# Performance work log

Measured on AMD Instinct MI355X. Metric: run time of the kernel, lower is better.

## Reference

```python
import jax, jax.numpy as jnp
import numpy as np

D = 128      # internal_dimensions
L = 4        # num_edge_convs
N = 100000   # nodes
E = 800000   # edges
G = 64       # graphs
IN = 4       # in_channels


def _ln(x, g, b):
    m = jnp.mean(x, -1, keepdims=True)
    v = jnp.mean((x - m) ** 2, -1, keepdims=True)
    return (x - m) * jax.lax.rsqrt(v + 1e-5) * g + b


def _gelu(x):
    return jax.nn.gelu(x, approximate=False)  # torch nn.GELU default (erf)


def _seg_mean(x, seg, n):
    s = jax.ops.segment_sum(x, seg, num_segments=n)
    c = jax.ops.segment_sum(jnp.ones((x.shape[0], 1), x.dtype), seg, num_segments=n)
    return s / jnp.maximum(c, 1.0)


def _seg_max(x, seg, n):
    m = jax.ops.segment_max(x, seg, num_segments=n)
    return jnp.where(jnp.isfinite(m), m, 0.0)  # empty segments -> 0 (PyG convention)


def _forward(x, edge_index, batch, num_graphs,
             in_W1, in_b1, in_g1, in_bn1, in_W2, in_b2, in_g2, in_bn2,
             pre_g, pre_b, cW1, cb1, cg1, cbb1, cW2, cb2, cg2, cbb2, pW, pb,
             ag_g, ag_b,
             kW1, kb1, kg1, kbb1, kW2, kb2, kg2, kbb2,
             kW3, kb3, kg3, kbb3, kW4, kb4):
    n = x.shape[0]
    # input_net: Linear -> LN -> GELU -> Linear -> LN   (dropout=0, eval)
    h = _gelu(_ln(x @ in_W1 + in_b1, in_g1, in_bn1))
    h = _ln(h @ in_W2 + in_b2, in_g2, in_bn2)

    x_in_max = _seg_max(h, batch, num_graphs)
    x_in_mean = _seg_mean(h, batch, num_graphs)

    src, dst = edge_index[0], edge_index[1]  # PyG: message from src (x_j) to dst (x_i)
    xcur = h
    for l in range(L):
        identity = xcur
        hn = _ln(xcur, pre_g[l], pre_b[l])
        xi = hn[dst]            # [E, D]
        xj = hn[src]            # [E, D]
        m = jnp.concatenate([xi, xj - xi], axis=-1)       # [E, 2D]
        m = _gelu(_ln(m @ cW1[l] + cb1[l], cg1[l], cbb1[l]))
        m = _gelu(_ln(m @ cW2[l] + cb2[l], cg2[l], cbb2[l]))
        a_max = _seg_max(m, dst, n)
        a_mean = _seg_mean(m, dst, n)
        aggr = jnp.concatenate([a_max, a_mean], axis=-1)  # [N, 2D]
        xcur = identity + aggr @ pW[l] + pb[l]

    xcur = _ln(xcur, ag_g, ag_b)
    x_g_max = _seg_max(xcur, batch, num_graphs)
    x_g_mean = _seg_mean(xcur, batch, num_graphs)

    xp = jnp.concatenate([x_in_max, x_in_mean, x_g_max, x_g_mean], axis=-1)  # [G, 4D]
    z = _gelu(_ln(xp @ kW1 + kb1, kg1, kbb1))
    z = _gelu(_ln(z @ kW2 + kb2, kg2, kbb2))
    z = _gelu(_ln(z @ kW3 + kb3, kg3, kbb3))
    return z @ kW4 + kb4  # [G, 1]


def setup_inputs() -> dict:
    key = jax.random.key(0)
    ks = iter(jax.random.split(key, 64))
    def W(shape, fan):
        return jax.random.normal(next(ks), shape, jnp.float32) * np.float32((2.0 / fan) ** 0.5)
    inp = {}
    inp["x"] = jax.random.normal(next(ks), (N, IN), jnp.float32)
    inp["edge_index"] = jax.random.randint(next(ks), (2, E), 0, N)
    inp["batch"] = jnp.sort(jax.random.randint(next(ks), (N,), 0, G))
    inp["num_graphs"] = G
    inp["in_W1"] = W((IN, D), IN); inp["in_b1"] = jnp.zeros((D,), jnp.float32)
    inp["in_g1"] = jnp.ones((D,), jnp.float32); inp["in_bn1"] = jnp.zeros((D,), jnp.float32)
    inp["in_W2"] = W((D, D), D); inp["in_b2"] = jnp.zeros((D,), jnp.float32)
    inp["in_g2"] = jnp.ones((D,), jnp.float32); inp["in_bn2"] = jnp.zeros((D,), jnp.float32)
    inp["pre_g"] = jnp.ones((L, D), jnp.float32); inp["pre_b"] = jnp.zeros((L, D), jnp.float32)
    inp["cW1"] = W((L, 2 * D, D), 2 * D); inp["cb1"] = jnp.zeros((L, D), jnp.float32)
    inp["cg1"] = jnp.ones((L, D), jnp.float32); inp["cbb1"] = jnp.zeros((L, D), jnp.float32)
    inp["cW2"] = W((L, D, D), D); inp["cb2"] = jnp.zeros((L, D), jnp.float32)
    inp["cg2"] = jnp.ones((L, D), jnp.float32); inp["cbb2"] = jnp.zeros((L, D), jnp.float32)
    inp["pW"] = W((L, 2 * D, D), 2 * D); inp["pb"] = jnp.zeros((L, D), jnp.float32)
    inp["ag_g"] = jnp.ones((D,), jnp.float32); inp["ag_b"] = jnp.zeros((D,), jnp.float32)
    inp["kW1"] = W((4 * D, D), 4 * D); inp["kb1"] = jnp.zeros((D,), jnp.float32)
    inp["kg1"] = jnp.ones((D,), jnp.float32); inp["kbb1"] = jnp.zeros((D,), jnp.float32)
    inp["kW2"] = W((D, D), D); inp["kb2"] = jnp.zeros((D,), jnp.float32)
    inp["kg2"] = jnp.ones((D,), jnp.float32); inp["kbb2"] = jnp.zeros((D,), jnp.float32)
    inp["kW3"] = W((D, D // 4), D); inp["kb3"] = jnp.zeros((D // 4,), jnp.float32)
    inp["kg3"] = jnp.ones((D // 4,), jnp.float32); inp["kbb3"] = jnp.zeros((D // 4,), jnp.float32)
    inp["kW4"] = W((D // 4, 1), D // 4); inp["kb4"] = jnp.zeros((1,), jnp.float32)
    return inp


def reference(x, edge_index, batch, num_graphs,
              in_W1, in_b1, in_g1, in_bn1, in_W2, in_b2, in_g2, in_bn2,
              pre_g, pre_b, cW1, cb1, cg1, cbb1, cW2, cb2, cg2, cbb2, pW, pb,
              ag_g, ag_b,
              kW1, kb1, kg1, kbb1, kW2, kb2, kg2, kbb2,
              kW3, kb3, kg3, kbb3, kW4, kb4):
    return _forward(x, edge_index, batch, num_graphs,
                    in_W1, in_b1, in_g1, in_bn1, in_W2, in_b2, in_g2, in_bn2,
                    pre_g, pre_b, cW1, cb1, cg1, cbb1, cW2, cb2, cg2, cbb2, pW, pb,
                    ag_g, ag_b,
                    kW1, kb1, kg1, kbb1, kW2, kb2, kg2, kbb2,
                    kW3, kb3, kg3, kbb3, kW4, kb4)
```

## Files before the change

kernel.cpp:

```cpp
#include <hip/hip_runtime.h>
#include <hip/hip_bf16.h>
#include <math.h>

__device__ __forceinline__ float geluf(float x) {
    return 0.5f * x * (1.0f + erff(x * 0.70710678118654752f));
}
#define MAPNEGINF 0x007FFFFFu
__device__ __forceinline__ float funmap(unsigned m) {
    return __uint_as_float((m & 0x80000000u) ? (m ^ 0x80000000u) : ~m);
}
__device__ __forceinline__ unsigned fmap(float f) {
    unsigned u = __float_as_uint(f);
    return ((int)u < 0) ? ~u : (u | 0x80000000u);
}
__device__ __forceinline__ float wred64(float v) {
#pragma unroll
    for (int m = 1; m < 64; m <<= 1) v += __shfl_xor(v, m);
    return v;
}
__device__ __forceinline__ unsigned short bf16r(float f) {
    unsigned u = __float_as_uint(f);
    u += 0x7fffu + ((u >> 16) & 1u);
    return (unsigned short)(u >> 16);
}
// ... 35 lines not shown
__global__ void k_zero(unsigned* __restrict__ p, int n) {
    const int i = blockIdx.x * 256 + threadIdx.x;
    if (i < n) p[i] = 0u;
}

__global__ void k_copyu(const unsigned* __restrict__ a, const unsigned* __restrict__ b,
                        unsigned* __restrict__ ac, unsigned* __restrict__ bc, int n) {
    const int i = blockIdx.x * 256 + threadIdx.x;
    if (i < n) {
        ac[i] = a[i];
        bc[i] = b[i];
    }
}

__global__ void k_count(const int* __restrict__ ei, unsigned* __restrict__ deg, int E) {
    const int e = blockIdx.x * 256 + threadIdx.x;
    if (e < E) atomicAdd(deg + ei[E + e], 1u);
}

__global__ void k_scan1(const unsigned* __restrict__ deg, unsigned* __restrict__ excl,
                        unsigned* __restrict__ bsum, int n) {
    __shared__ unsigned sh[256];
    const int t = threadIdx.x;
    const int base = blockIdx.x * 1024 + t * 4;
    unsigned v0 = (base + 0 < n) ? deg[base + 0] : 0u;
    unsigned v1 = (base + 1 < n) ? deg[base + 1] : 0u;
    unsigned v2 = (base + 2 < n) ? deg[base + 2] : 0u;
    unsigned v3 = (base + 3 < n) ? deg[base + 3] : 0u;
    const unsigned s = v0 + v1 + v2 + v3;
    sh[t] = s;
    __syncthreads();
    for (int off = 1; off < 256; off <<= 1) {
        unsigned x = 0;
        if (t >= off) x = sh[t - off];
        __syncthreads();
        if (t >= off) sh[t] += x;
        __syncthreads();
    }
    const unsigned ebase = sh[t] - s;
    if (base + 0 < n) excl[base + 0] = ebase;
    if (base + 1 < n) excl[base + 1] = ebase + v0;
    if (base + 2 < n) excl[base + 2] = ebase + v0 + v1;
    if (base + 3 < n) excl[base + 3] = ebase + v0 + v1 + v2;
    if (t == 255) bsum[blockIdx.x] = sh[255];
}

__global__ void k_scan2(unsigned* __restrict__ bsum, int nb) {
    __shared__ unsigned sh[256];
    const int t = threadIdx.x;
    const unsigned v = (t < nb) ? bsum[t] : 0u;
    sh[t] = v;
    __syncthreads();
    for (int off = 1; off < 256; off <<= 1) {
        unsigned x = 0;
        if (t >= off) x = sh[t - off];
        __syncthreads();
        if (t >= off) sh[t] += x;
        __syncthreads();
    }
    if (t < nb) bsum[t] = sh[t] - v;
}

__global__ void k_scan3(unsigned* __restrict__ excl, const unsigned* __restrict__ bsum, int n) {
    const int t = threadIdx.x;
    const int base = blockIdx.x * 1024 + t * 4;
    const unsigned add = bsum[blockIdx.x];
#pragma unroll
    for (int j = 0; j < 4; ++j)
        if (base + j < n) excl[base + j] += add;
}

__global__ void k_scatter(const int* __restrict__ ei, unsigned* __restrict__ cursor,
                          int* __restrict__ esrc, int* __restrict__ edst, int E) {
    const int e = blockIdx.x * 256 + threadIdx.x;
    if (e < E) {
        const int s = ei[e];
        const int d = ei[E + e];
        const unsigned pos = atomicAdd(cursor + d, 1u);
        esrc[pos] = s;
        edst[pos] = d;
    }
}

__global__ void k_in1(const float* __restrict__ x, const float* __restrict__ W1,
                      const float* __restrict__ b1, const float* __restrict__ g1,
                      const float* __restrict__ bn1, float* __restrict__ h, int n) {
    const int t = threadIdx.x, lane = t & 63, wave = t >> 6;
    const int d0 = lane << 1;
    const float2 w0 = *(const float2*)(W1 + d0);
    const float2 w1 = *(const float2*)(W1 + 128 + d0);
    const float2 w2 = *(const float2*)(W1 + 256 + d0);
    const float2 w3 = *(const float2*)(W1 + 384 + d0);
    const float2 bb = *(const float2*)(b1 + d0);
    const float2 gg = *(const float2*)(g1 + d0);
    const float2 nn = *(const float2*)(bn1 + d0);
    const int stride = gridDim.x * 4;
    for (int node = blockIdx.x * 4 + wave; node < n; node += stride) {
        const float4 xv = *(const float4*)(x + (size_t)node * 4);
        float h0 = bb.x + xv.x * w0.x + xv.y * w1.x + xv.z * w2.x + xv.w * w3.x;
        float h1 = bb.y + xv.x * w0.y + xv.y * w1.y + xv.z * w2.y + xv.w * w3.y;
        const float s = wred64(h0 + h1), q = wred64(h0 * h0 + h1 * h1);
        const float mean = s * 0.0078125f, var = q * 0.0078125f - mean * mean;
        const float rs = rsqrtf(var + 1e-5f);
        h0 = geluf((h0 - mean) * rs * gg.x + nn.x);
        h1 = geluf((h1 - mean) * rs * gg.y + nn.y);
        *(float2*)(h + (size_t)node * 128 + d0) = make_float2(h0, h1);
    }
}

__global__ __launch_bounds__(256, 2) void k_in2(const float* __restrict__ A,
                                                const float* __restrict__ W,
                                                const float* __restrict__ bias,
                                                const float* __restrict__ g,
                                                const float* __restrict__ b,
                                                float* __restrict__ C, int n) {
    __shared__ float As[64 * 132];
    __shared__ float Ws[4096];
    const int t = threadIdx.x;
    const int n0 = blockIdx.x * 64;
    {
        const int r = t >> 2, c0 = (t & 3) << 5;
        const int row = n0 + r;
        const bool ok = row < n;
#pragma unroll
        for (int j = 0; j < 8; ++j) {
            const int col = c0 + (j << 2);
            float4 v = make_float4(0.f, 0.f, 0.f, 0.f);
            if (ok) v = *(const float4*)(A + (size_t)row * 128 + col);
            *(float4*)(As + r * 132 + col) = v;
        }
    }
    float acc[4][8];
#pragma unroll
    for (int r = 0; r < 4; ++r)
#pragma unroll
        for (int o = 0; o < 8; ++o) acc[r][o] = 0.f;
    const int og = t & 15, eg = t >> 4;
    const int ogc = og << 2, r0 = eg << 2;
#pragma unroll
    for (int q4 = 0; q4 < 4; ++q4) {
        stage_wq(Ws, W + q4 * 4096, t);
        __syncthreads();
        kloop_q(As, Ws, acc, r0, ogc, q4 * 32);
        __syncthreads();
    }
    const float4 bA = *(const float4*)(bias + ogc);
    const float4 bB = *(const float4*)(bias + 64 + ogc);
    const float4 gA = *(const float4*)(g + ogc);
    const float4 gB = *(const float4*)(g + 64 + ogc);
    const float4 lA = *(const float4*)(b + ogc);
    const float4 lB = *(const float4*)(b + 64 + ogc);
#pragma unroll
    for (int r = 0; r < 4; ++r) {
        float v[8];
        v[0] = acc[r][0] + bA.x; v[1] = acc[r][1] + bA.y;
        v[2] = acc[r][2] + bA.z; v[3] = acc[r][3] + bA.w;
        v[4] = acc[r][4] + bB.x; v[5] = acc[r][5] + bB.y;
        v[6] = acc[r][6] + bB.z; v[7] = acc[r][7] + bB.w;
        float s = 0.f, q = 0.f;
#pragma unroll
        for (int o = 0; o < 8; ++o) { s += v[o]; q += v[o] * v[o]; }
#pragma unroll
        for (int m = 1; m < 16; m <<= 1) { s += __shfl_xor(s, m); q += __shfl_xor(q, m); }
        const float mean = s * 0.0078125f;
        const float var = q * 0.0078125f - mean * mean;
        const float rs = rsqrtf(var + 1e-5f);
        const int row = n0 + r0 + r;
        if (row < n) {
            *(float4*)(C + (size_t)row * 128 + ogc) = make_float4(
                (v[0] - mean) * rs * gA.x + lA.x, (v[1] - mean) * rs * gA.y + lA.y,
                (v[2] - mean) * rs * gA.z + lA.z, (v[3] - mean) * rs * gA.w + lA.w);
            *(float4*)(C + (size_t)row * 128 + 64 + ogc) = make_float4(
                (v[4] - mean) * rs * gB.x + lB.x, (v[5] - mean) * rs * gB.y + lB.y,
                (v[6] - mean) * rs * gB.z + lB.z, (v[7] - mean) * rs * gB.w + lB.w);
        }
    }
}

__global__ void k_ln(const float* __restrict__ in, const float* __restrict__ g,
                     const float* __restrict__ b, float* __restrict__ out, int n) {
    const int t = threadIdx.x, lane = t & 63, wave = t >> 6;
    const int d0 = lane << 1;
    const float ga = g[d0], gb = g[d0 + 1], ba = b[d0], bb = b[d0 + 1];
    const int stride = gridDim.x * 4;
    for (int node = blockIdx.x * 4 + wave; node < n; node += stride) {
        const float2 v = *(const float2*)(in + (size_t)node * 128 + d0);
        const float s = wred64(v.x + v.y), q = wred64(v.x * v.x + v.y * v.y);
        const float mean = s * 0.0078125f, var = q * 0.0078125f - mean * mean;
        const float rs = rsqrtf(var + 1e-5f);
        *(float2*)(out + (size_t)node * 128 + d0) =
            make_float2((v.x - mean) * rs * ga + ba, (v.y - mean) * rs * gb + bb);
    }
}

__global__ void k_wxj(const float* __restrict__ c, float* __restrict__ Wx,
                      float* __restrict__ Wj) {
    const int idx = blockIdx.x * 256 + threadIdx.x;
    const float a = c[idx], b = c[16384 + idx];
    Wx[idx] = a - b;
    Wj[idx] = b;
}

__global__ __launch_bounds__(256, 2) void k_gemmh(const float* __restrict__ A,
                                                  const float* __restrict__ W,
                                                  const float* __restrict__ bias,
                                                  unsigned short* __restrict__ C, int n) {
    __shared__ float As[64 * 132];
    __shared__ float Ws[4096];
    const int t = threadIdx.x;
    const int n0 = blockIdx.x * 64;
    {
        const int r = t >> 2, c0 = (t & 3) << 5;
        const int row = n0 + r;
        const bool ok = row < n;
#pragma unroll
        for (int j = 0; j < 8; ++j) {
            const int col = c0 + (j << 2);
            float4 v = make_float4(0.f, 0.f, 0.f, 0.f);
            if (ok) v = *(const float4*)(A + (size_t)row * 128 + col);
            *(float4*)(As + r * 132 + col) = v;
        }
    }
    float acc[4][8];
#pragma unroll
    for (int r = 0; r < 4; ++r)
#pragma unroll
        for (int o = 0; o < 8; ++o) acc[r][o] = 0.f;
    const int og = t & 15, eg = t >> 4;
    const int ogc = og << 2, r0 = eg << 2;
#pragma unroll
    for (int q4 = 0; q4 < 4; ++q4) {
        stage_wq(Ws, W + q4 * 4096, t);
        __syncthreads();
        kloop_q(As, Ws, acc, r0, ogc, q4 * 32);
        __syncthreads();
    }
    float4 bA = make_float4(0.f, 0.f, 0.f, 0.f), bB = bA;
    if (bias) {
        bA = *(const float4*)(bias + ogc);
        bB = *(const float4*)(bias + 64 + ogc);
    }
#pragma unroll
    for (int r = 0; r < 4; ++r) {
        const int row = n0 + r0 + r;
        if (row < n) {
            ushort4 u0, u1;
            u0.x = bf16r(acc[r][0] + bA.x); u0.y = bf16r(acc[r][1] + bA.y);
            u0.z = bf16r(acc[r][2] + bA.z); u0.w = bf16r(acc[r][3] + bA.w);
            u1.x = bf16r(acc[r][4] + bB.x); u1.y = bf16r(acc[r][5] + bB.y);
            u1.z = bf16r(acc[r][6] + bB.z); u1.w = bf16r(acc[r][7] + bB.w);
            *(ushort4*)(C + (size_t)row * 128 + ogc) = u0;
            *(ushort4*)(C + (size_t)row * 128 + 64 + ogc) = u1;
        }
    }
}

__global__ __launch_bounds__(256, 2) void k_edge(
    const unsigned short* __restrict__ P, const unsigned short* __restrict__ Q,
    const int* __restrict__ esrc, const int* __restrict__ edst, const float* __restrict__ W2,
    const float* __restrict__ g1, const float* __restrict__ b1, const float* __restrict__ cb2,
    const float* __restrict__ g2, const float* __restrict__ b2,
    const unsigned* __restrict__ rowend, const unsigned* __restrict__ degc,
    float* __restrict__ amax, float* __restrict__ asum, float* __restrict__ recmax,
    float* __restrict__ recsum, int* __restrict__ recid, int E) {
    __shared__ float Us[64 * 132];
    __shared__ float Ws[4096];
    __shared__ int sdst[64], ssrc[64], sdg[64];
    __shared__ float scb2[128], sg2[128], sb2[128];
    const int t = threadIdx.x;
    const int base = blockIdx.x * 512;
    if (t >= 128) {
        const int d = t - 128;
        scb2[d] = cb2[d];
        sg2[d] = g2[d];
        sb2[d] = b2[d];
    }
    const int lane = t & 63, wave = t >> 6;
    const int d0 = lane << 1;
    const float g1a = g1[d0], g1b = g1[d0 + 1], b1a = b1[d0], b1b = b1[d0 + 1];
    const int og = t & 15, eg = t >> 4;
    const int ogc = og << 2, r0 = eg << 2;
    int cur = -1, istart = 0;
    float vmax = -INFINITY, vsum = 0.f;
    int id0 = -1, id1 = -1;

    for (int s8 = 0; s8 < 8; ++s8) {
        const int sb = base + s8 * 64;
        __syncthreads();
        if (t < 64) {
            const int idx = sb + t;
            const int ci = idx < E ? idx : (E - 1);
            ssrc[t] = esrc[ci];
            const int d = edst[ci];
            sdg[t] = d;
            sdst[t] = (idx < E) ? d : -1;
        }
        __syncthreads();
#pragma unroll 4
        for (int p = 0; p < 16; ++p) {
            const int i = (p << 2) + wave;
            const unsigned pu = *(const unsigned*)(P + ((size_t)sdg[i] << 7) + d0);
            const unsigned qu = *(const unsigned*)(Q + ((size_t)ssrc[i] << 7) + d0);
            const float x0 = __uint_as_float(pu << 16) + __uint_as_float(qu << 16);
            const float x1 =
                __uint_as_float(pu & 0xffff0000u) + __uint_as_float(qu & 0xffff0000u);
            const float s = wred64(x0 + x1);
            const float q = wred64(x0 * x0 + x1 * x1);
            const float mean = s * 0.0078125f;
            const float var = q * 0.0078125f - mean * mean;
            const float rs = rsqrtf(var + 1e-5f);
            const float y0 = geluf((x0 - mean) * rs * g1a + b1a);
            const float y1 = geluf((x1 - mean) * rs * g1b + b1b);
            *(float2*)(Us + i * 132 + d0) = make_float2(y0, y1);
        }
        float acc[4][8];
#pragma unroll
        for (int r = 0; r < 4; ++r)
#pragma unroll
            for (int o = 0; o < 8; ++o) acc[r][o] = 0.f;
#pragma unroll
        for (int q4 = 0; q4 < 4; ++q4) {
            stage_wq(Ws, W2 + q4 * 4096, t);
            __syncthreads();
            kloop_q(Us, Ws, acc, r0, ogc, q4 * 32);
            __syncthreads();
        }
#pragma unroll
        for (int r = 0; r < 4; ++r) {
            float v[8];
            float s = 0.f, q = 0.f;
#pragma unroll
            for (int o = 0; o < 8; ++o) {
                const int col = (o < 4) ? (ogc + o) : (64 + ogc + o - 4);
                v[o] = acc[r][o] + scb2[col];
                s += v[o];
                q += v[o] * v[o];
            }
#pragma unroll
            for (int m = 1; m < 16; m <<= 1) { s += __shfl_xor(s, m); q += __shfl_xor(q, m); }
            const float mean = s * 0.0078125f;
            const float var = q * 0.0078125f - mean * mean;
            const float rs = rsqrtf(var + 1e-5f);
#pragma unroll
            for (int o = 0; o < 8; ++o) {
                const int col = (o < 4) ? (ogc + o) : (64 + ogc + o - 4);
                v[o] = geluf((v[o] - mean) * rs * sg2[col] + sb2[col]);
            }
            *(float4*)(Us + (r0 + r) * 132 + ogc) = make_float4(v[0], v[1], v[2], v[3]);
            *(float4*)(Us + (r0 + r) * 132 + 64 + ogc) = make_float4(v[4], v[5], v[6], v[7]);
        }
        __syncthreads();
        if (t < 128) {
            for (int i = 0; i < 64; ++i) {
                const int dn = sdst[i];
                const int gi = s8 * 64 + i;
                if (dn != cur) {
                    if (cur >= 0) {
                        const unsigned re = rowend[cur];
                        const unsigned rs0 = re - degc[cur];
                        const unsigned ps = (unsigned)(base + istart);
                        const unsigned pe = (unsigned)(base + gi);
                        if (ps == rs0 && pe == re) {
                            amax[(size_t)cur * 128 + t] = vmax;
                            asum[(size_t)cur * 128 + t] = vsum;
                        } else {
                            const int slot = (istart == 0) ? 0 : 1;
                            const size_t ro = (size_t)(2 * blockIdx.x + slot) * 128 + t;
                            recmax[ro] = vmax;
                            recsum[ro] = vsum;
                            if (slot == 0) id0 = cur; else id1 = cur;
                        }
                    }
                    cur = dn;
                    istart = gi;
                    vmax = -INFINITY;
                    vsum = 0.f;
                }
                if (dn >= 0) {
                    const float v = Us[i * 132 + t];
                    vmax = fmaxf(vmax, v);
                    vsum += v;
                }
            }
        }
    }
    if (t < 128 && cur >= 0) {
        const int iend = min(512, E - base);
        const unsigned re = rowend[cur];
        const unsigned rs0 = re - degc[cur];
        const unsigned ps = (unsigned)(base + istart);
        const unsigned pe = (unsigned)(base + iend);
        if (ps == rs0 && pe == re) {
            amax[(size_t)cur * 128 + t] = vmax;
            asum[(size_t)cur * 128 + t] = vsum;
        } else {
            const int slot = (istart == 0) ? 0 : 1;
            const size_t ro = (size_t)(2 * blockIdx.x + slot) * 128 + t;
            recmax[ro] = vmax;
            recsum[ro] = vsum;
            if (slot == 0) id0 = cur; else id1 = cur;
        }
    }
    if (t == 0) {
        recid[2 * blockIdx.x] = id0;
        recid[2 * blockIdx.x + 1] = id1;
    }
}

__global__ void k_merge(const unsigned* __restrict__ rowend, const unsigned* __restrict__ degc,
                        const float* __restrict__ recmax, const float* __restrict__ recsum,
                        const int* __restrict__ recid, float* __restrict__ amax,
                        float* __restrict__ asum, int n) {
    const int node = blockIdx.x * 2 + (threadIdx.x >> 7);
    const int t = threadIdx.x & 127;
    if (node >= n) return;
    const unsigned dg = degc[node];
    if (dg == 0u) {
        amax[(size_t)node * 128 + t] = 0.f;
        asum[(size_t)node * 128 + t] = 0.f;
        return;
    }
    const unsigned re = rowend[node], rs = re - dg;
    const int b0 = rs >> 9, b1 = (re - 1) >> 9;
    if (b0 == b1) return;
    float m = -INFINITY, s = 0.f;
    for (int b = b0; b <= b1; ++b) {
#pragma unroll
        for (int sl = 0; sl < 2; ++sl) {
            if (recid[2 * b + sl] == node) {
                const size_t ro = (size_t)(2 * b + sl) * 128 + t;
                m = fmaxf(m, recmax[ro]);
                s += recsum[ro];
            }
        }
    }
    amax[(size_t)node * 128 + t] = m;
    asum[(size_t)node * 128 + t] = s;
}

__global__ __launch_bounds__(256, 2) void k_update(const float* __restrict__ amax,
                                                   const float* __restrict__ asum,
                                                   const unsigned* __restrict__ degc,
                                                   const float* __restrict__ pW,
                                                   const float* __restrict__ pb,
                                                   float* __restrict__ xcur, int n) {
    __shared__ float As[64 * 132];
    __shared__ float Ws[4096];
    const int t = threadIdx.x;
    const int n0 = blockIdx.x * 64;
    const int og = t & 15, eg = t >> 4;
    const int ogc = og << 2, r0 = eg << 2;
    float acc[4][8];
#pragma unroll
    for (int r = 0; r < 4; ++r)
#pragma unroll
        for (int o = 0; o < 8; ++o) acc[r][o] = 0.f;
    const int r = t >> 2, c0 = (t & 3) << 5;
    const int row = n0 + r;
    const bool ok = row < n;
#pragma unroll
    for (int pass = 0; pass < 2; ++pass) {
        if (pass == 0) {
#pragma unroll
            for (int j = 0; j < 8; ++j) {
                const int col = c0 + (j << 2);
                float4 v = make_float4(0.f, 0.f, 0.f, 0.f);
                if (ok) v = *(const float4*)(amax + (size_t)row * 128 + col);
                *(float4*)(As + r * 132 + col) = v;
            }
        } else {
            float inv = 0.f;
            if (ok) {
                const unsigned dv = degc[row];
                inv = 1.f / (float)(dv < 1u ? 1u : dv);
            }
#pragma unroll
            for (int j = 0; j < 8; ++j) {
                const int col = c0 + (j << 2);
                float4 v = make_float4(0.f, 0.f, 0.f, 0.f);
                if (ok) {
                    const float4 sv = *(const float4*)(asum + (size_t)row * 128 + col);
                    v = make_float4(sv.x * inv, sv.y * inv, sv.z * inv, sv.w * inv);
                }
                *(float4*)(As + r * 132 + col) = v;
            }
        }
#pragma unroll
        for (int q4 = 0; q4 < 4; ++q4) {
            stage_wq(Ws, pW + (size_t)(pass * 128 + q4 * 32) * 128, t);
            __syncthreads();
            kloop_q(As, Ws, acc, r0, ogc, q4 * 32);
            __syncthreads();
        }
    }
    const float4 bA = *(const float4*)(pb + ogc);
    const float4 bB = *(const float4*)(pb + 64 + ogc);
#pragma unroll
    for (int rr = 0; rr < 4; ++rr) {
        const int orow = n0 + r0 + rr;
        if (orow < n) {
            const float4 x0 = *(const float4*)(xcur + (size_t)orow * 128 + ogc);
            const float4 x1 = *(const float4*)(xcur + (size_t)orow * 128 + 64 + ogc);
            *(float4*)(xcur + (size_t)orow * 128 + ogc) =
                make_float4(x0.x + acc[rr][0] + bA.x, x0.y + acc[rr][1] + bA.y,
                            x0.z + acc[rr][2] + bA.z, x0.w + acc[rr][3] + bA.w);
            *(float4*)(xcur + (size_t)orow * 128 + 64 + ogc) =
                make_float4(x1.x + acc[rr][4] + bB.x, x1.y + acc[rr][5] + bB.y,
                            x1.z + acc[rr][6] + bB.z, x1.w + acc[rr][7] + bB.w);
        }
    }
}

__global__ void k_pool_init(unsigned* __restrict__ gmax1, float* __restrict__ gsum1,
                            unsigned* __restrict__ gcount1, unsigned* __restrict__ gmax2,
                            float* __restrict__ gsum2, unsigned* __restrict__ gcount2, int ng) {
    const int i = blockIdx.x * 256 + threadIdx.x;
    if (i < ng * 128) {
        gmax1[i] = MAPNEGINF;
        gsum1[i] = 0.f;
        gmax2[i] = MAPNEGINF;
        gsum2[i] = 0.f;
    }
    if (i < ng) {
        gcount1[i] = 0u;
        gcount2[i] = 0u;
    }
}

__global__ void k_pool(const float* __restrict__ in, const int* __restrict__ batch,
                       unsigned* __restrict__ gmax, float* __restrict__ gsum,
                       unsigned* __restrict__ gcount, int n) {
    const int t = threadIdx.x;
    if (t >= 128) return;
    const int per = (n + gridDim.x - 1) / gridDim.x;
    const int i0 = blockIdx.x * per;
    const int i1 = min(n, i0 + per);
    if (i0 >= i1) return;
    int cur = batch[i0];
    float vmax = -INFINITY, vsum = 0.f;
    unsigned cnt = 0;
    for (int i = i0; i < i1; ++i) {
        const int g = batch[i];
        if (g != cur) {
            atomicMax(gmax + (size_t)cur * 128 + t, fmap(vmax));
            atomicAdd(gsum + (size_t)cur * 128 + t, vsum);
            if (t == 0) atomicAdd(gcount + cur, cnt);
            cur = g;
            vmax = -INFINITY;
            vsum = 0.f;
            cnt = 0;
        }
        const float v = in[(size_t)i * 128 + t];
        vmax = fmaxf(vmax, v);
        vsum += v;
        cnt++;
    }
    atomicMax(gmax + (size_t)cur * 128 + t, fmap(vmax));
    atomicAdd(gsum + (size_t)cur * 128 + t, vsum);
    if (t == 0) atomicAdd(gcount + cur, cnt);
}

__global__ void k_xp(const unsigned* __restrict__ gmax1, const float* __restrict__ gsum1,
                     const unsigned* __restrict__ gcount1, const unsigned* __restrict__ gmax2,
                     const float* __restrict__ gsum2, const unsigned* __restrict__ gcount2,
                     float* __restrict__ xp) {
    const int g = blockIdx.x, d = threadIdx.x;
    const unsigned c1u = gcount1[g], c2u = gcount2[g];
    const float c1 = (float)(c1u < 1u ? 1u : c1u);
    const float c2 = (float)(c2u < 1u ? 1u : c2u);
    const unsigned m1 = gmax1[g * 128 + d], m2 = gmax2[g * 128 + d];
    xp[g * 512 + d] = (m1 == MAPNEGINF) ? 0.f : funmap(m1);
    xp[g * 512 + 128 + d] = gsum1[g * 128 + d] / c1;
    xp[g * 512 + 256 + d] = (m2 == MAPNEGINF) ? 0.f : funmap(m2);
    xp[g * 512 + 384 + d] = gsum2[g * 128 + d] / c2;
}

__global__ __launch_bounds__(64) void k_know(
    const float* __restrict__ xp, const float* __restrict__ kW1, const float* __restrict__ kb1,
    const float* __restrict__ kg1, const float* __restrict__ kbb1, const float* __restrict__ kW2,
    const float* __restrict__ kb2, const float* __restrict__ kg2, const float* __restrict__ kbb2,
    const float* __restrict__ kW3, const float* __restrict__ kb3, const float* __restrict__ kg3,
    const float* __restrict__ kbb3, const float* __restrict__ kW4, const float* __restrict__ kb4,
    float* __restrict__ out) {
    __shared__ float sh[512];
    __shared__ float s3[32];
    const int l = threadIdx.x, g = blockIdx.x;
    const int d0 = l << 1;
    *(float4*)(sh + l * 8) = *(const float4*)(xp + g * 512 + l * 8);
    *(float4*)(sh + l * 8 + 4) = *(const float4*)(xp + g * 512 + l * 8 + 4);
    __syncthreads();
    float a0 = kb1[d0], a1 = kb1[d0 + 1];
    for (int k = 0; k < 512; ++k) {
// ... 42 lines not shown
    {
        float s = c0 + c1, q = c0 * c0 + c1 * c1;
#pragma unroll
        for (int m = 1; m < 16; m <<= 1) {
            s += __shfl_xor(s, m);
            q += __shfl_xor(q, m);
        }
        const float mean = s * 0.03125f, var = q * 0.03125f - mean * mean;
        const float rs = rsqrtf(var + 1e-5f);
        c0 = geluf((c0 - mean) * rs * kg3[d3] + kbb3[d3]);
        c1 = geluf((c1 - mean) * rs * kg3[d3 + 1] + kbb3[d3 + 1]);
    }
    if (l < 16) {
        s3[d3] = c0;
        s3[d3 + 1] = c1;
    }
    __syncthreads();
    if (l == 0) {
        float rr = kb4[0];
        for (int k = 0; k < 32; ++k) rr += s3[k] * kW4[k];
        out[g] = rr;
    }
}

extern "C" void kernel_launch(void* const* d_in, const int* in_sizes, int n_in, void* d_out,
                              int out_size, void* d_ws, size_t ws_size, hipStream_t stream) {
    const int N = in_sizes[0] / 4;
    const int E = in_sizes[1] / 2;
    const int G = 64;
    const int L = 4;

    const float* x = (const float*)d_in[0];
    const int* ei = (const int*)d_in[1];
    const int* batch = (const int*)d_in[2];
    const float* inW1 = (const float*)d_in[4];
    const float* inb1 = (const float*)d_in[5];
    const float* ing1 = (const float*)d_in[6];
    const float* inbn1 = (const float*)d_in[7];
    const float* inW2 = (const float*)d_in[8];
    const float* inb2 = (const float*)d_in[9];
    const float* ing2 = (const float*)d_in[10];
    const float* inbn2 = (const float*)d_in[11];
    const float* pre_g = (const float*)d_in[12];
    const float* pre_b = (const float*)d_in[13];
    const float* cW1 = (const float*)d_in[14];
    const float* cb1 = (const float*)d_in[15];
    const float* cg1 = (const float*)d_in[16];
    const float* cbb1 = (const float*)d_in[17];
    const float* cW2 = (const float*)d_in[18];
    const float* cb2 = (const float*)d_in[19];
    const float* cg2 = (const float*)d_in[20];
    const float* cbb2 = (const float*)d_in[21];
    const float* pW = (const float*)d_in[22];
    const float* pb = (const float*)d_in[23];
    const float* ag_g = (const float*)d_in[24];
    const float* ag_b = (const float*)d_in[25];
    const float* kW1 = (const float*)d_in[26];
    const float* kb1 = (const float*)d_in[27];
    const float* kg1 = (const float*)d_in[28];
    const float* kbb1 = (const float*)d_in[29];
    const float* kW2 = (const float*)d_in[30];
    const float* kb2 = (const float*)d_in[31];
    const float* kg2 = (const float*)d_in[32];
    const float* kbb2 = (const float*)d_in[33];
    const float* kW3 = (const float*)d_in[34];
    const float* kb3 = (const float*)d_in[35];
    const float* kg3 = (const float*)d_in[36];
    const float* kbb3 = (const float*)d_in[37];
    const float* kW4 = (const float*)d_in[38];
    const float* kb4 = (const float*)d_in[39];
    float* out = (float*)d_out;

    const int nblkE = (E + 511) / 512;

    char* wsb = (char*)d_ws;
    size_t off = 0;
    auto ALC = [&](size_t bytes) {
        void* p = wsb + off;
        off = (off + bytes + 255) & ~(size_t)255;
        return p;
    };
    const size_t NB = (size_t)N * 128 * 4;
    float* xcur = (float*)ALC(NB);
    float* hn = (float*)ALC(NB);
    float* amax = hn;
    float* asum = (float*)ALC(NB);
    unsigned short* Pb = (unsigned short*)ALC((size_t)N * 128 * 2);
    unsigned short* Qb = (unsigned short*)ALC((size_t)N * 128 * 2);
    unsigned* deg = (unsigned*)ALC((size_t)N * 4);
    unsigned* cursor = (unsigned*)ALC((size_t)N * 4);
    unsigned* degc = (unsigned*)ALC((size_t)N * 4);
    unsigned* rowend = (unsigned*)ALC((size_t)N * 4);
    unsigned* bsum = (unsigned*)ALC(4096);
    int* esrc = (int*)ALC((size_t)E * 4);
    int* edst = (int*)ALC((size_t)E * 4);
    float* recmax = (float*)ALC((size_t)nblkE * 2 * 128 * 4);
    float* recsum = (float*)ALC((size_t)nblkE * 2 * 128 * 4);
    int* recid = (int*)ALC((size_t)nblkE * 2 * 4);
    float* Wx = (float*)ALC(65536);
    float* Wj = (float*)ALC(65536);
    unsigned* gmax1 = (unsigned*)ALC((size_t)G * 128 * 4);
    float* gsum1 = (float*)ALC((size_t)G * 128 * 4);
    unsigned* gcount1 = (unsigned*)ALC((size_t)G * 4);
    unsigned* gmax2 = (unsigned*)ALC((size_t)G * 128 * 4);
    float* gsum2 = (float*)ALC((size_t)G * 128 * 4);
    unsigned* gcount2 = (unsigned*)ALC((size_t)G * 4);
    float* xp = (float*)ALC((size_t)G * 512 * 4);

    if (off > ws_size) {
        k_zero<<<(out_size + 255) / 256, 256, 0, stream>>>((unsigned*)d_out, out_size);
        return;
    }

    k_zero<<<(N + 255) / 256, 256, 0, stream>>>(deg, N);
    k_count<<<(E + 255) / 256, 256, 0, stream>>>(ei, deg, E);
    const int nb = (N + 1023) / 1024;
    k_scan1<<<nb, 256, 0, stream>>>(deg, cursor, bsum, N);
    k_scan2<<<1, 256, 0, stream>>>(bsum, nb);
    k_scan3<<<nb, 256, 0, stream>>>(cursor, bsum, N);
    k_scatter<<<(E + 255) / 256, 256, 0, stream>>>(ei, cursor, esrc, edst, E);
    k_copyu<<<(N + 255) / 256, 256, 0, stream>>>(deg, cursor, degc, rowend, N);

    const int gemmGrid = (N + 63) / 64;
    k_in1<<<1024, 256, 0, stream>>>(x, inW1, inb1, ing1, inbn1, hn, N);
    k_in2<<<gemmGrid, 256, 0, stream>>>(hn, inW2, inb2, ing2, inbn2, xcur, N);
    k_pool_init<<<(G * 128 + 255) / 256, 256, 0, stream>>>(gmax1, gsum1, gcount1, gmax2, gsum2,
                                                           gcount2, G);
    k_pool<<<512, 256, 0, stream>>>(xcur, batch, gmax1, gsum1, gcount1, N);

    for (int l = 0; l < L; ++l) {
        k_wxj<<<64, 256, 0, stream>>>(cW1 + (size_t)l * 32768, Wx, Wj);
        k_ln<<<1024, 256, 0, stream>>>(xcur, pre_g + l * 128, pre_b + l * 128, hn, N);
        k_gemmh<<<gemmGrid, 256, 0, stream>>>(hn, Wx, cb1 + l * 128, Pb, N);
        k_gemmh<<<gemmGrid, 256, 0, stream>>>(hn, Wj, (const float*)nullptr, Qb, N);
        k_edge<<<nblkE, 256, 0, stream>>>(Pb, Qb, esrc, edst, cW2 + (size_t)l * 16384,
                                          cg1 + l * 128, cbb1 + l * 128, cb2 + l * 128,
                                          cg2 + l * 128, cbb2 + l * 128, rowend, degc, amax, asum,
                                          recmax, recsum, recid, E);
        k_merge<<<(N + 1) / 2, 256, 0, stream>>>(rowend, degc, recmax, recsum, recid, amax, asum,
                                                 N);
        k_update<<<gemmGrid, 256, 0, stream>>>(amax, asum, degc, pW + (size_t)l * 32768,
                                               pb + l * 128, xcur, N);
    }

    k_ln<<<1024, 256, 0, stream>>>(xcur, ag_g, ag_b, hn, N);
    k_pool<<<512, 256, 0, stream>>>(hn, batch, gmax2, gsum2, gcount2, N);
    k_xp<<<G, 128, 0, stream>>>(gmax1, gsum1, gcount1, gmax2, gsum2, gcount2, xp);
    k_know<<<G, 64, 0, stream>>>(xp, kW1, kb1, kg1, kbb1, kW2, kb2, kg2, kbb2, kW3, kb3, kg3,
                                 kbb3, kW4, kb4, out);
}
```

Before: 95.78 ms.

## Fuse input MLP, pre-LN with both P/Q GEMMs, and aggregation projection

Merges the two input-net kernels into one, computing the first linear layer, LayerNorm and GELU straight into shared memory before the second GEMM. Folds the per-layer LayerNorm and the weight split (Wx/Wj) into a single kernel that computes both P and Q from one staged activation tile. Moves the post-aggregation projection into the edge kernel and the merge kernel as per-node matrix-vector products, leaving a simple elementwise residual add. This cuts launches and intermediate N×128 buffers, but replaces a tiled GEMM with per-node matvecs that re-read the projection weights for every node and add block-wide barriers per destination run.

```diff
diff --git a/kernel.cpp b/kernel.cpp
--- a/kernel.cpp
+++ b/kernel.cpp
@@ -141,52 +141,48 @@
     }
 }
 
-__global__ void k_in1(const float* __restrict__ x, const float* __restrict__ W1,
-                      const float* __restrict__ b1, const float* __restrict__ g1,
-                      const float* __restrict__ bn1, float* __restrict__ h, int n) {
-    const int t = threadIdx.x, lane = t & 63, wave = t >> 6;
-    const int d0 = lane << 1;
-    const float2 w0 = *(const float2*)(W1 + d0);
-    const float2 w1 = *(const float2*)(W1 + 128 + d0);
-    const float2 w2 = *(const float2*)(W1 + 256 + d0);
-    const float2 w3 = *(const float2*)(W1 + 384 + d0);
-    const float2 bb = *(const float2*)(b1 + d0);
-    const float2 gg = *(const float2*)(g1 + d0);
-    const float2 nn = *(const float2*)(bn1 + d0);
-    const int stride = gridDim.x * 4;
-    for (int node = blockIdx.x * 4 + wave; node < n; node += stride) {
-        const float4 xv = *(const float4*)(x + (size_t)node * 4);
-        float h0 = bb.x + xv.x * w0.x + xv.y * w1.x + xv.z * w2.x + xv.w * w3.x;
-        float h1 = bb.y + xv.x * w0.y + xv.y * w1.y + xv.z * w2.y + xv.w * w3.y;
-        const float s = wred64(h0 + h1), q = wred64(h0 * h0 + h1 * h1);
-        const float mean = s * 0.0078125f, var = q * 0.0078125f - mean * mean;
-        const float rs = rsqrtf(var + 1e-5f);
-        h0 = geluf((h0 - mean) * rs * gg.x + nn.x);
-        h1 = geluf((h1 - mean) * rs * gg.y + nn.y);
-        *(float2*)(h + (size_t)node * 128 + d0) = make_float2(h0, h1);
-    }
-}
-
-__global__ __launch_bounds__(256, 2) void k_in2(const float* __restrict__ A,
-                                                const float* __restrict__ W,
-                                                const float* __restrict__ bias,
-                                                const float* __restrict__ g,
-                                                const float* __restrict__ b,
-                                                float* __restrict__ C, int n) {
+__global__ void k_in(const float* __restrict__ x, const float* __restrict__ W1,
+                     const float* __restrict__ b1, const float* __restrict__ g1,
+                     const float* __restrict__ bn1, const float* __restrict__ W2,
+                     const float* __restrict__ b2, const float* __restrict__ g2,
+                     const float* __restrict__ bn2, float* __restrict__ C, int n) {
     __shared__ float As[64 * 132];
     __shared__ float Ws[4096];
+    __shared__ float W1s[512];
     const int t = threadIdx.x;
     const int n0 = blockIdx.x * 64;
+    if (t < 128) {
+        W1s[t] = W1[t];
+        W1s[128 + t] = W1[128 + t];
+        W1s[256 + t] = W1[256 + t];
+        W1s[384 + t] = W1[384 + t];
+    }
+    __syncthreads();
     {
         const int r = t >> 2, c0 = (t & 3) << 5;
         const int row = n0 + r;
-        const bool ok = row < n;
-#pragma unroll
-        for (int j = 0; j < 8; ++j) {
-            const int col = c0 + (j << 2);
-            float4 v = make_float4(0.f, 0.f, 0.f, 0.f);
-            if (ok) v = *(const float4*)(A + (size_t)row * 128 + col);
-            *(float4*)(As + r * 132 + col) = v;
+        float4 xv = make_float4(0.f, 0.f, 0.f, 0.f);
+        if (row < n) xv = *(const float4*)(x + (size_t)row * 4);
+        float hv[32];
+        float s = 0.f, q = 0.f;
+#pragma unroll
+        for (int j = 0; j < 32; ++j) {
+            const int c = c0 + j;
+            const float z = b1[c] + xv.x * W1s[c] + xv.y * W1s[128 + c] +
+                            xv.z * W1s[256 + c] + xv.w * W1s[384 + c];
+            hv[j] = z;
+            s += z;
+            q += z * z;
+        }
+        s += __shfl_xor(s, 1); s += __shfl_xor(s, 2);
+        q += __shfl_xor(q, 1); q += __shfl_xor(q, 2);
+        const float mean = s * 0.0078125f;
+        const float var = q * 0.0078125f - mean * mean;
+        const float rs = rsqrtf(var + 1e-5f);
+#pragma unroll
+        for (int j = 0; j < 32; ++j) {
+            const int c = c0 + j;
+            As[r * 132 + c] = geluf((hv[j] - mean) * rs * g1[c] + bn1[c]);
         }
     }
     float acc[4][8];
@@ -198,17 +194,17 @@
     const int ogc = og << 2, r0 = eg << 2;
 #pragma unroll
     for (int q4 = 0; q4 < 4; ++q4) {
-        stage_wq(Ws, W + q4 * 4096, t);
+        stage_wq(Ws, W2 + q4 * 4096, t);
         __syncthreads();
         kloop_q(As, Ws, acc, r0, ogc, q4 * 32);
         __syncthreads();
     }
-    const float4 bA = *(const float4*)(bias + ogc);
-    const float4 bB = *(const float4*)(bias + 64 + ogc);
-    const float4 gA = *(const float4*)(g + ogc);
-    const float4 gB = *(const float4*)(g + 64 + ogc);
-    const float4 lA = *(const float4*)(b + ogc);
-    const float4 lB = *(const float4*)(b + 64 + ogc);
+    const float4 bA = *(const float4*)(b2 + ogc);
+    const float4 bB = *(const float4*)(b2 + 64 + ogc);
+    const float4 gA = *(const float4*)(g2 + ogc);
+    const float4 gB = *(const float4*)(g2 + 64 + ogc);
+    const float4 lA = *(const float4*)(bn2 + ogc);
+    const float4 lB = *(const float4*)(bn2 + 64 + ogc);
 #pragma unroll
     for (int r = 0; r < 4; ++r) {
         float v[8];
@@ -252,64 +248,90 @@
     }
 }
 
-__global__ void k_wxj(const float* __restrict__ c, float* __restrict__ Wx,
-                      float* __restrict__ Wj) {
-    const int idx = blockIdx.x * 256 + threadIdx.x;
-    const float a = c[idx], b = c[16384 + idx];
-    Wx[idx] = a - b;
-    Wj[idx] = b;
-}
-
-__global__ __launch_bounds__(256, 2) void k_gemmh(const float* __restrict__ A,
-                                                  const float* __restrict__ W,
-                                                  const float* __restrict__ bias,
-                                                  unsigned short* __restrict__ C, int n) {
+__global__ void k_pq2(const float* __restrict__ xcur, const float* __restrict__ g,
+                      const float* __restrict__ b, const float* __restrict__ cW1,
+                      const float* __restrict__ cb1, unsigned short* __restrict__ P,
+                      unsigned short* __restrict__ Q, int n) {
     __shared__ float As[64 * 132];
     __shared__ float Ws[4096];
+    __shared__ float sg[128], sb[128];
     const int t = threadIdx.x;
     const int n0 = blockIdx.x * 64;
+    if (t < 128) { sg[t] = g[t]; sb[t] = b[t]; }
+    __syncthreads();
     {
         const int r = t >> 2, c0 = (t & 3) << 5;
         const int row = n0 + r;
         const bool ok = row < n;
+        float4 v4[8];
+        float s = 0.f, q = 0.f;
+        if (ok) {
+#pragma unroll
+            for (int j = 0; j < 8; ++j) {
+                v4[j] = *(const float4*)(xcur + (size_t)row * 128 + c0 + (j << 2));
+                s += v4[j].x + v4[j].y + v4[j].z + v4[j].w;
+                q += v4[j].x * v4[j].x + v4[j].y * v4[j].y + v4[j].z * v4[j].z +
+                     v4[j].w * v4[j].w;
+            }
+        } else {
+#pragma unroll
+            for (int j = 0; j < 8; ++j) v4[j] = make_float4(0.f, 0.f, 0.f, 0.f);
+        }
+        s += __shfl_xor(s, 1); s += __shfl_xor(s, 2);
+        q += __shfl_xor(q, 1); q += __shfl_xor(q, 2);
+        const float mean = s * 0.0078125f;
+        const float var = q * 0.0078125f - mean * mean;
+        const float rs = rsqrtf(var + 1e-5f);
 #pragma unroll
         for (int j = 0; j < 8; ++j) {
-            const int col = c0 + (j << 2);
-            float4 v = make_float4(0.f, 0.f, 0.f, 0.f);
-            if (ok) v = *(const float4*)(A + (size_t)row * 128 + col);
-            *(float4*)(As + r * 132 + col) = v;
-        }
-    }
-    float acc[4][8];
+            const int c = c0 + (j << 2);
+            As[r * 132 + c + 0] = (v4[j].x - mean) * rs * sg[c + 0] + sb[c + 0];
+            As[r * 132 + c + 1] = (v4[j].y - mean) * rs * sg[c + 1] + sb[c + 1];
+            As[r * 132 + c + 2] = (v4[j].z - mean) * rs * sg[c + 2] + sb[c + 2];
+            As[r * 132 + c + 3] = (v4[j].w - mean) * rs * sg[c + 3] + sb[c + 3];
+        }
+    }
+    float accP[4][8], accQ[4][8];
 #pragma unroll
     for (int r = 0; r < 4; ++r)
 #pragma unroll
-        for (int o = 0; o < 8; ++o) acc[r][o] = 0.f;
+        for (int o = 0; o < 8; ++o) { accP[r][o] = 0.f; accQ[r][o] = 0.f; }
     const int og = t & 15, eg = t >> 4;
     const int ogc = og << 2, r0 = eg << 2;
 #pragma unroll
     for (int q4 = 0; q4 < 4; ++q4) {
-        stage_wq(Ws, W + q4 * 4096, t);
-        __syncthreads();
-        kloop_q(As, Ws, acc, r0, ogc, q4 * 32);
-        __syncthreads();
-    }
-    float4 bA = make_float4(0.f, 0.f, 0.f, 0.f), bB = bA;
-    if (bias) {
-        bA = *(const float4*)(bias + ogc);
-        bB = *(const float4*)(bias + 64 + ogc);
-    }
+        stage_wq(Ws, cW1 + q4 * 4096, t);
+        __syncthreads();
+        kloop_q(As, Ws, accP, r0, ogc, q4 * 32);
+        __syncthreads();
+        stage_wq(Ws, cW1 + 16384 + q4 * 4096, t);
+        __syncthreads();
+        kloop_q(As, Ws, accQ, r0, ogc, q4 * 32);
+        __syncthreads();
+    }
+    const float4 bA = *(const float4*)(cb1 + ogc);
+    const float4 bB = *(const float4*)(cb1 + 64 + ogc);
 #pragma unroll
     for (int r = 0; r < 4; ++r) {
         const int row = n0 + r0 + r;
         if (row < n) {
-            ushort4 u0, u1;
-            u0.x = bf16r(acc[r][0] + bA.x); u0.y = bf16r(acc[r][1] + bA.y);
-            u0.z = bf16r(acc[r][2] + bA.z); u0.w = bf16r(acc[r][3] + bA.w);
-            u1.x = bf16r(acc[r][4] + bB.x); u1.y = bf16r(acc[r][5] + bB.y);
-            u1.z = bf16r(acc[r][6] + bB.z); u1.w = bf16r(acc[r][7] + bB.w);
-            *(ushort4*)(C + (size_t)row * 128 + ogc) = u0;
-            *(ushort4*)(C + (size_t)row * 128 + 64 + ogc) = u1;
+            ushort4 p0, p1, q0, q1;
+            p0.x = bf16r(accP[r][0] - accQ[r][0] + bA.x);
+            p0.y = bf16r(accP[r][1] - accQ[r][1] + bA.y);
+            p0.z = bf16r(accP[r][2] - accQ[r][2] + bA.z);
+            p0.w = bf16r(accP[r][3] - accQ[r][3] + bA.w);
+            p1.x = bf16r(accP[r][4] - accQ[r][4] + bB.x);
+            p1.y = bf16r(accP[r][5] - accQ[r][5] + bB.y);
+            p1.z = bf16r(accP[r][6] - accQ[r][6] + bB.z);
+            p1.w = bf16r(accP[r][7] - accQ[r][7] + bB.w);
+            q0.x = bf16r(accQ[r][0]); q0.y = bf16r(accQ[r][1]);
+            q0.z = bf16r(accQ[r][2]); q0.w = bf16r(accQ[r][3]);
+            q1.x = bf16r(accQ[r][4]); q1.y = bf16r(accQ[r][5]);
+            q1.z = bf16r(accQ[r][6]); q1.w = bf16r(accQ[r][7]);
+            *(ushort4*)(P + (size_t)row * 128 + ogc) = p0;
+            *(ushort4*)(P + (size_t)row * 128 + 64 + ogc) = p1;
+            *(ushort4*)(Q + (size_t)row * 128 + ogc) = q0;
+            *(ushort4*)(Q + (size_t)row * 128 + 64 + ogc) = q1;
         }
     }
 }
@@ -320,12 +342,13 @@
     const float* __restrict__ g1, const float* __restrict__ b1, const float* __restrict__ cb2,
     const float* __restrict__ g2, const float* __restrict__ b2,
     const unsigned* __restrict__ rowend, const unsigned* __restrict__ degc,
-    float* __restrict__ amax, float* __restrict__ asum, float* __restrict__ recmax,
+    const float* __restrict__ pW, float* __restrict__ upd, float* __restrict__ recmax,
     float* __restrict__ recsum, int* __restrict__ recid, int E) {
     __shared__ float Us[64 * 132];
     __shared__ float Ws[4096];
     __shared__ int sdst[64], ssrc[64], sdg[64];
     __shared__ float scb2[128], sg2[128], sb2[128];
+    __shared__ float smx[128], ssm[128], spart[256];
     const int t = threadIdx.x;
     const int base = blockIdx.x * 512;
     if (t >= 128) {
@@ -342,6 +365,39 @@
     int cur = -1, istart = 0;
     float vmax = -INFINITY, vsum = 0.f;
     int id0 = -1, id1 = -1;
+
+    auto flushrun = [&](int iend) {
+        const unsigned re = rowend[cur];
+        const unsigned dg = degc[cur];
+        const unsigned rs0 = re - dg;
+        const unsigned ps = (unsigned)(base + istart), pe = (unsigned)(base + iend);
+        if (ps == rs0 && pe == re) {
+            if (t < 128) {
+                smx[t] = vmax;
+                ssm[t] = vsum / (float)dg;
+            }
+            __syncthreads();
+            {
+                const int d = t & 127;
+                const float* wc = pW + ((t >> 7) ? 16384 : 0) + d;
+                const float* sv = (t >> 7) ? ssm : smx;
+                float a = 0.f;
+#pragma unroll 8
+                for (int k = 0; k < 128; ++k) a += sv[k] * wc[(size_t)k << 7];
+                spart[t] = a;
+            }
+            __syncthreads();
+            if (t < 128) upd[(size_t)cur * 128 + t] = spart[t] + spart[t + 128];
+        } else {
+            const int slot = (istart == 0) ? 0 : 1;
+            if (t < 128) {
+                const size_t ro = (size_t)(2 * blockIdx.x + slot) * 128 + t;
+                recmax[ro] = vmax;
+                recsum[ro] = vsum;
+            }
+            if (slot == 0) id0 = cur; else id1 = cur;
+        }
+    };
 
     for (int s8 = 0; s8 < 8; ++s8) {
         const int sb = base + s8 * 64;
@@ -409,74 +465,41 @@
             *(float4*)(Us + (r0 + r) * 132 + 64 + ogc) = make_float4(v[4], v[5], v[6], v[7]);
         }
         __syncthreads();
-        if (t < 128) {
-            for (int i = 0; i < 64; ++i) {
-                const int dn = sdst[i];
-                const int gi = s8 * 64 + i;
-                if (dn != cur) {
-                    if (cur >= 0) {
-                        const unsigned re = rowend[cur];
-                        const unsigned rs0 = re - degc[cur];
-                        const unsigned ps = (unsigned)(base + istart);
-                        const unsigned pe = (unsigned)(base + gi);
-                        if (ps == rs0 && pe == re) {
-                            amax[(size_t)cur * 128 + t] = vmax;
-                            asum[(size_t)cur * 128 + t] = vsum;
-                        } else {
-                            const int slot = (istart == 0) ? 0 : 1;
-                            const size_t ro = (size_t)(2 * blockIdx.x + slot) * 128 + t;
-                            recmax[ro] = vmax;
-                            recsum[ro] = vsum;
-                            if (slot == 0) id0 = cur; else id1 = cur;
-                        }
-                    }
-                    cur = dn;
-                    istart = gi;
-                    vmax = -INFINITY;
-                    vsum = 0.f;
-                }
-                if (dn >= 0) {
-                    const float v = Us[i * 132 + t];
-                    vmax = fmaxf(vmax, v);
-                    vsum += v;
-                }
+        for (int i = 0; i < 64; ++i) {
+            const int dn = sdst[i];
+            const int gi = s8 * 64 + i;
+            if (dn != cur) {
+                if (cur >= 0) flushrun(gi);
+                cur = dn;
+                istart = gi;
+                vmax = -INFINITY;
+                vsum = 0.f;
             }
-        }
-    }
-    if (t < 128 && cur >= 0) {
-        const int iend = min(512, E - base);
-        const unsigned re = rowend[cur];
-        const unsigned rs0 = re - degc[cur];
-        const unsigned ps = (unsigned)(base + istart);
-        const unsigned pe = (unsigned)(base + iend);
-        if (ps == rs0 && pe == re) {
-            amax[(size_t)cur * 128 + t] = vmax;
-            asum[(size_t)cur * 128 + t] = vsum;
-        } else {
-            const int slot = (istart == 0) ? 0 : 1;
-            const size_t ro = (size_t)(2 * blockIdx.x + slot) * 128 + t;
-            recmax[ro] = vmax;
-            recsum[ro] = vsum;
-            if (slot == 0) id0 = cur; else id1 = cur;
-        }
-    }
+            if (dn >= 0 && t < 128) {
+                const float v = Us[i * 132 + t];
+                vmax = fmaxf(vmax, v);
+                vsum += v;
+            }
+        }
+    }
+    if (cur >= 0) flushrun(min(512, E - base));
     if (t == 0) {
         recid[2 * blockIdx.x] = id0;
         recid[2 * blockIdx.x + 1] = id1;
     }
 }
 
-__global__ void k_merge(const unsigned* __restrict__ rowend, const unsigned* __restrict__ degc,
-                        const float* __restrict__ recmax, const float* __restrict__ recsum,
-                        const int* __restrict__ recid, float* __restrict__ amax,
-                        float* __restrict__ asum, int n) {
-    const int node = blockIdx.x * 2 + (threadIdx.x >> 7);
-    const int t = threadIdx.x & 127;
+__global__ void k_merge2(const unsigned* __restrict__ rowend, const unsigned* __restrict__ degc,
+                         const float* __restrict__ recmax, const float* __restrict__ recsum,
+                         const int* __restrict__ recid, const float* __restrict__ pW,
+                         float* __restrict__ upd, int n) {
+    __shared__ float sm[128], ss[128];
+    const int node = blockIdx.x;
+    const int d = threadIdx.x;
     if (node >= n) return;
     const unsigned dg = degc[node];
     if (dg == 0u) {
-        amax[(size_t)node * 128 + t] = 0.f;
-        asum[(size_t)node * 128 + t] = 0.f;
+        upd[(size_t)node * 128 + d] = 0.f;
         return;
     }
     const unsigned re = rowend[node], rs = re - dg;
@@ -487,86 +510,32 @@
 #pragma unroll
         for (int sl = 0; sl < 2; ++sl) {
             if (recid[2 * b + sl] == node) {
-                const size_t ro = (size_t)(2 * b + sl) * 128 + t;
+                const size_t ro = (size_t)(2 * b + sl) * 128 + d;
                 m = fmaxf(m, recmax[ro]);
                 s += recsum[ro];
             }
         }
     }
-    amax[(size_t)node * 128 + t] = m;
-    asum[(size_t)node * 128 + t] = s;
-}
-
-__global__ __launch_bounds__(256, 2) void k_update(const float* __restrict__ amax,
-                                                   const float* __restrict__ asum,
-                                                   const unsigned* __restrict__ degc,
-                                                   const float* __restrict__ pW,
-                                                   const float* __restrict__ pb,
-                                                   float* __restrict__ xcur, int n) {
-    __shared__ float As[64 * 132];
-    __shared__ float Ws[4096];
-    const int t = threadIdx.x;
-    const int n0 = blockIdx.x * 64;
-    const int og = t & 15, eg = t >> 4;
-    const int ogc = og << 2, r0 = eg << 2;
-    float acc[4][8];
-#pragma unroll
-    for (int r = 0; r < 4; ++r)
-#pragma unroll
-        for (int o = 0; o < 8; ++o) acc[r][o] = 0.f;
-    const int r = t >> 2, c0 = (t & 3) << 5;
-    const int row = n0 + r;
-    const bool ok = row < n;
-#pragma unroll
-    for (int pass = 0; pass < 2; ++pass) {
-        if (pass == 0) {
-#pragma unroll
-            for (int j = 0; j < 8; ++j) {
-                const int col = c0 + (j << 2);
-                float4 v = make_float4(0.f, 0.f, 0.f, 0.f);
-                if (ok) v = *(const float4*)(amax + (size_t)row * 128 + col);
-                *(float4*)(As + r * 132 + col) = v;
-            }
-        } else {
-            float inv = 0.f;
-            if (ok) {
-                const unsigned dv = degc[row];
-                inv = 1.f / (float)(dv < 1u ? 1u : dv);
-            }
-#pragma unroll
-            for (int j = 0; j < 8; ++j) {
-                const int col = c0 + (j << 2);
-                float4 v = make_float4(0.f, 0.f, 0.f, 0.f);
-                if (ok) {
-                    const float4 sv = *(const float4*)(asum + (size_t)row * 128 + col);
-                    v = make_float4(sv.x * inv, sv.y * inv, sv.z * inv, sv.w * inv);
-                }
-                *(float4*)(As + r * 132 + col) = v;
-            }
-        }
-#pragma unroll
-        for (int q4 = 0; q4 < 4; ++q4) {
-            stage_wq(Ws, pW + (size_t)(pass * 128 + q4 * 32) * 128, t);
-            __syncthreads();
-            kloop_q(As, Ws, acc, r0, ogc, q4 * 32);
-            __syncthreads();
-        }
-    }
-    const float4 bA = *(const float4*)(pb + ogc);
-    const float4 bB = *(const float4*)(pb + 64 + ogc);
-#pragma unroll
-    for (int rr = 0; rr < 4; ++rr) {
-        const int orow = n0 + r0 + rr;
-        if (orow < n) {
-            const float4 x0 = *(const float4*)(xcur + (size_t)orow * 128 + ogc);
-            const float4 x1 = *(const float4*)(xcur + (size_t)orow * 128 + 64 + ogc);
-            *(float4*)(xcur + (size_t)orow * 128 + ogc) =
-                make_float4(x0.x + acc[rr][0] + bA.x, x0.y + acc[rr][1] + bA.y,
-                            x0.z + acc[rr][2] + bA.z, x0.w + acc[rr][3] + bA.w);
-            *(float4*)(xcur + (size_t)orow * 128 + 64 + ogc) =
-                make_float4(x1.x + acc[rr][4] + bB.x, x1.y + acc[rr][5] + bB.y,
-                            x1.z + acc[rr][6] + bB.z, x1.w + acc[rr][7] + bB.w);
-        }
+    sm[d] = m;
+    ss[d] = s / (float)dg;
+    __syncthreads();
+    float a = 0.f;
+#pragma unroll 8
+    for (int k = 0; k < 128; ++k)
+        a += sm[k] * pW[(size_t)k * 128 + d] + ss[k] * pW[(size_t)(128 + k) * 128 + d];
+    upd[(size_t)node * 128 + d] = a;
+}
+
+__global__ void k_updS(const float* __restrict__ upd, const float* __restrict__ pb,
+                       float* __restrict__ xcur, int n32) {
+    for (int i = blockIdx.x * 256 + threadIdx.x; i < n32; i += gridDim.x * 256) {
+        const int c4 = (i & 31) << 2;
+        const float4 u = ((const float4*)upd)[i];
+        const float4 pv = *(const float4*)(pb + c4);
+        const float4 xv = ((const float4*)xcur)[i];
+        ((float4*)xcur)[i] =
+            make_float4(xv.x + u.x + pv.x, xv.y + u.y + pv.y, xv.z + u.z + pv.z,
+                        xv.w + u.w + pv.w);
     }
 }
 
@@ -775,9 +744,7 @@
     };
     const size_t NB = (size_t)N * 128 * 4;
     float* xcur = (float*)ALC(NB);
-    float* hn = (float*)ALC(NB);
-    float* amax = hn;
-    float* asum = (float*)ALC(NB);
+    float* upd = (float*)ALC(NB);
     unsigned short* Pb = (unsigned short*)ALC((size_t)N * 128 * 2);
     unsigned short* Qb = (unsigned short*)ALC((size_t)N * 128 * 2);
     unsigned* deg = (unsigned*)ALC((size_t)N * 4);
@@ -790,8 +757,6 @@
     float* recmax = (float*)ALC((size_t)nblkE * 2 * 128 * 4);
     float* recsum = (float*)ALC((size_t)nblkE * 2 * 128 * 4);
     int* recid = (int*)ALC((size_t)nblkE * 2 * 4);
-    float* Wx = (float*)ALC(65536);
-    float* Wj = (float*)ALC(65536);
     unsigned* gmax1 = (unsigned*)ALC((size_t)G * 128 * 4);
     float* gsum1 = (float*)ALC((size_t)G * 128 * 4);
     unsigned* gcount1 = (unsigned*)ALC((size_t)G * 4);
@@ -814,30 +779,27 @@
     k_scatter<<<(E + 255) / 256, 256, 0, stream>>>(ei, cursor, esrc, edst, E);
     k_copyu<<<(N + 255) / 256, 256, 0, stream>>>(deg, cursor, degc, rowend, N);
 
-    const int gemmGrid = (N + 63) / 64;
-    k_in1<<<1024, 256, 0, stream>>>(x, inW1, inb1, ing1, inbn1, hn, N);
-    k_in2<<<gemmGrid, 256, 0, stream>>>(hn, inW2, inb2, ing2, inbn2, xcur, N);
+    const int grid64 = (N + 63) / 64;
+    k_in<<<grid64, 256, 0, stream>>>(x, inW1, inb1, ing1, inbn1, inW2, inb2, ing2, inbn2, xcur,
+                                     N);
     k_pool_init<<<(G * 128 + 255) / 256, 256, 0, stream>>>(gmax1, gsum1, gcount1, gmax2, gsum2,
                                                            gcount2, G);
     k_pool<<<512, 256, 0, stream>>>(xcur, batch, gmax1, gsum1, gcount1, N);
 
     for (int l = 0; l < L; ++l) {
-        k_wxj<<<64, 256, 0, stream>>>(cW1 + (size_t)l * 32768, Wx, Wj);
-        k_ln<<<1024, 256, 0, stream>>>(xcur, pre_g + l * 128, pre_b + l * 128, hn, N);
-        k_gemmh<<<gemmGrid, 256, 0, stream>>>(hn, Wx, cb1 + l * 128, Pb, N);
-        k_gemmh<<<gemmGrid, 256, 0, stream>>>(hn, Wj, (const float*)nullptr, Qb, N);
+        k_pq2<<<grid64, 256, 0, stream>>>(xcur, pre_g + l * 128, pre_b + l * 128,
+                                          cW1 + (size_t)l * 32768, cb1 + l * 128, Pb, Qb, N);
         k_edge<<<nblkE, 256, 0, stream>>>(Pb, Qb, esrc, edst, cW2 + (size_t)l * 16384,
                                           cg1 + l * 128, cbb1 + l * 128, cb2 + l * 128,
-                                          cg2 + l * 128, cbb2 + l * 128, rowend, degc, amax, asum,
-                                          recmax, recsum, recid, E);
-        k_merge<<<(N + 1) / 2, 256, 0, stream>>>(rowend, degc, recmax, recsum, recid, amax, asum,
-                                                 N);
-        k_update<<<gemmGrid, 256, 0, stream>>>(amax, asum, degc, pW + (size_t)l * 32768,
-                                               pb + l * 128, xcur, N);
-    }
-
-    k_ln<<<1024, 256, 0, stream>>>(xcur, ag_g, ag_b, hn, N);
-    k_pool<<<512, 256, 0, stream>>>(hn, batch, gmax2, gsum2, gcount2, N);
+                                          cg2 + l * 128, cbb2 + l * 128, rowend, degc,
+                                          pW + (size_t)l * 32768, upd, recmax, recsum, recid, E);
+        k_merge2<<<N, 128, 0, stream>>>(rowend, degc, recmax, recsum, recid,
+                                        pW + (size_t)l * 32768, upd, N);
+        k_updS<<<2048, 256, 0, stream>>>(upd, pb + l * 128, xcur, N * 32);
+    }
+
+    k_ln<<<1024, 256, 0, stream>>>(xcur, ag_g, ag_b, upd, N);
+    k_pool<<<512, 256, 0, stream>>>(upd, batch, gmax2, gsum2, gcount2, N);
     k_xp<<<G, 128, 0, stream>>>(gmax1, gsum1, gcount1, gmax2, gsum2, gcount2, xp);
     k_know<<<G, 64, 0, stream>>>(xp, kW1, kb1, kg1, kbb1, kW2, kb2, kg2, kbb2, kW3, kb3, kg3,
                                  kbb3, kW4, kb4, out);
```

After: 82.25 ms. -14.1%, faster.
